# Kernel tuning notes

Measured on AMD Instinct MI355X. Metric: run time of the kernel, lower is better.

## Reference

```python
import jax, jax.numpy as jnp
import numpy as np

N = 100000      # nodes
E = 1600000     # edges
G = 256         # graphs in batch
D_IN = 92
D = 64          # out_dim
EPS = 1e-5      # batchnorm eps


def setup_inputs() -> dict:
    key = jax.random.key(0)
    ks = jax.random.split(key, 20)

    def lin_w(k, fan_in, fan_out):
        return jax.random.normal(k, (fan_in, fan_out), jnp.float32) / np.sqrt(fan_in).astype(np.float32)

    inp = {
        "x": jax.random.normal(ks[0], (N, D_IN), jnp.float32),
        "edge_index": jax.random.randint(ks[1], (2, E), 0, N, dtype=jnp.int64),
        "edge_weight": jax.random.uniform(ks[2], (E,), jnp.float32),
        "batch": jnp.sort(jax.random.randint(ks[3], (N,), 0, G, dtype=jnp.int64)),
        # GCNConv layer 0 (in_channels -> out_dim) + BatchNorm
        "W0": lin_w(ks[4], D_IN, D), "b0": jnp.zeros((D,), jnp.float32),
        "g0": jnp.ones((D,), jnp.float32), "beta0": jnp.zeros((D,), jnp.float32),
        # GCNConv layers 1,2 (out_dim -> out_dim) + BatchNorms
        "W1": lin_w(ks[5], D, D), "b1": jnp.zeros((D,), jnp.float32),
        "g1": jnp.ones((D,), jnp.float32), "beta1": jnp.zeros((D,), jnp.float32),
        "W2": lin_w(ks[6], D, D), "b2": jnp.zeros((D,), jnp.float32),
        "g2": jnp.ones((D,), jnp.float32), "beta2": jnp.zeros((D,), jnp.float32),
        # post MLP: Linear(out_dim,100) -> ReLU -> Linear(100,1)
        "Wp1": lin_w(ks[7], D, 100), "bp1": jnp.zeros((100,), jnp.float32),
        "Wp2": lin_w(ks[8], 100, 1), "bp2": jnp.zeros((1,), jnp.float32),
    }
    return inp


def reference(x, edge_index, edge_weight, batch,
              W0, b0, g0, beta0,
              W1, b1, g1, beta1,
              W2, b2, g2, beta2,
              Wp1, bp1, Wp2, bp2):
    n = x.shape[0]
    # --- gcn_norm with self-loops (fill weight 1), symmetric normalization ---
    loop = jnp.arange(n)
    row = jnp.concatenate([edge_index[0], loop])          # source nodes
    col = jnp.concatenate([edge_index[1], loop])          # target nodes
    w = jnp.concatenate([edge_weight, jnp.ones((n,), x.dtype)])
    deg = jax.ops.segment_sum(w, col, num_segments=n)
    dinv = jnp.where(deg > 0, deg ** -0.5, 0.0)
    norm = dinv[row] * w * dinv[col]                      # [E+N]

    def conv(h, W, b):
        h = h @ W                                         # [n, D]
        msg = norm[:, None] * h[row]                      # gather + scale
        return jax.ops.segment_sum(msg, col, num_segments=n) + b

    def bn(h, g, beta):  # training-mode batchnorm over node dim
        mu = h.mean(0)
        var = h.var(0)
        return (h - mu) * jax.lax.rsqrt(var + EPS) * g + beta

    h = jax.nn.relu(bn(conv(x, W0, b0), g0, beta0))
    h = jax.nn.relu(bn(conv(h, W1, b1), g1, beta1))
    h = jax.nn.relu(bn(conv(h, W2, b2), g2, beta2))

    # global_mean_pool over graph ids
    sums = jax.ops.segment_sum(h, batch, num_segments=G)
    cnt = jax.ops.segment_sum(jnp.ones((n,), h.dtype), batch, num_segments=G)
    pooled = sums / jnp.clip(cnt, 1.0)[:, None]           # [G, D]

    return jax.nn.relu(pooled @ Wp1 + bp1) @ Wp2 + bp2    # [G, 1]
```

## Files before the change

kernel.cpp:

```cpp
#include <hip/hip_runtime.h>
#include <hip/hip_bf16.h>

#define NGRAPH 256
#define BNEPS 1e-5f
#define SEGCAP 64
#define BSHIFT 9
#define BSPAN  512
#define BCAP   10240
#define BSTRIDE 16384
#define GSTAT  8192

typedef short s16x8 __attribute__((ext_vector_type(8)));
typedef float f32x4 __attribute__((ext_vector_type(4)));

__device__ __forceinline__ float bf2f(unsigned short u) {
    return __uint_as_float(((unsigned)u) << 16);
}
__device__ __forceinline__ unsigned short f2bf(float f) {
    unsigned u = __float_as_uint(f);
    unsigned r = (u + 0x7FFFu + ((u >> 16) & 1u)) >> 16;
    return (unsigned short)r;
}

__global__ __launch_bounds__(256) void k_part(const int* __restrict__ row, const int* __restrict__ col,
                                              const float* __restrict__ w,
                                              int* __restrict__ gcur,
                                              float2* __restrict__ stage, int E, int NB) {
    __shared__ int lhist[256];
    __shared__ int lbase[256];
    int tid = threadIdx.x;
    if (tid < NB) lhist[tid] = 0;
    __syncthreads();
    int c[8], lp[8];
    int base = blockIdx.x * 2048;
    #pragma unroll
    for (int k = 0; k < 8; ++k) {
        int e = base + k * 256 + tid;
        c[k] = (e < E) ? col[e] : -1;
        lp[k] = (c[k] >= 0) ? atomicAdd(&lhist[c[k] >> BSHIFT], 1) : 0;
    }
    __syncthreads();
    if (tid < NB && lhist[tid] > 0) lbase[tid] = atomicAdd(&gcur[tid], lhist[tid]);
    __syncthreads();
    #pragma unroll
    for (int k = 0; k < 8; ++k) {
        int e = base + k * 256 + tid;
        if (c[k] < 0) continue;
        int b = c[k] >> BSHIFT;
        int doff = c[k] & (BSPAN - 1);
        int src = row[e];
        float we = w[e];
        int pos = lbase[b] + lp[k];
        if (pos < BCAP)
            stage[(size_t)b * BCAP + pos] =
                make_float2(__int_as_float((doff << 17) | src), we);
    }
}

__global__ __launch_bounds__(256) void k_place(const int* __restrict__ gcur,
                                               const float2* __restrict__ stage,
                                               int* __restrict__ rowptr,
                                               int* __restrict__ cntArr,
                                               float2* __restrict__ edata,
                                               float* __restrict__ dinv, int N) {
    __shared__ int lhist[512];
    __shared__ int lexcl[512];
    __shared__ int lcur[512];
    __shared__ float lwsum[512];
    __shared__ int lts[256];
    int b = blockIdx.x;
    int tid = threadIdx.x;
    int cnt = min(gcur[b], BCAP);
    lhist[tid] = 0; lhist[tid + 256] = 0;
    lcur[tid] = 0;  lcur[tid + 256] = 0;
    lwsum[tid] = 0.0f; lwsum[tid + 256] = 0.0f;
    __syncthreads();
    for (int i = tid; i < cnt; i += 256) {
        unsigned u = __float_as_uint(stage[(size_t)b * BCAP + i].x);
        atomicAdd(&lhist[u >> 17], 1);
    }
    __syncthreads();
    int c0 = (lhist[2 * tid] + 7) & ~7;
    int c1 = (lhist[2 * tid + 1] + 7) & ~7;
    int tsum = c0 + c1;
    lts[tid] = tsum;
    __syncthreads();
    for (int o = 1; o < 256; o <<= 1) {
        int t = (tid >= o) ? lts[tid - o] : 0;
        __syncthreads();
        lts[tid] += t;
        __syncthreads();
    }
    int excl = lts[tid] - tsum;
    lexcl[2 * tid] = excl;
    lexcl[2 * tid + 1] = excl + c0;
    __syncthreads();
    int base = b * BSTRIDE;
    for (int i = tid; i < 512; i += 256) {
        int node = (b << BSHIFT) + i;
        if (node < N) { rowptr[node] = base + lexcl[i]; cntArr[node] = lhist[i]; }
    }
    for (int i = tid; i < cnt; i += 256) {
        float2 p = stage[(size_t)b * BCAP + i];
        unsigned u = __float_as_uint(p.x);
        int doff = (int)(u >> 17);
        int src  = (int)(u & 0x1FFFFu);
        int lp = atomicAdd(&lcur[doff], 1);
        atomicAdd(&lwsum[doff], p.y);
        int pos = lexcl[doff] + lp;
        if (pos < BSTRIDE)
            edata[(size_t)base + pos] = make_float2(__int_as_float(src), p.y);
    }
    __syncthreads();
    for (int i = tid; i < 512; i += 256) {
        int node = (b << BSHIFT) + i;
        if (node < N) dinv[node] = rsqrtf(1.0f + lwsum[i]);
        int c = lhist[i];
        int e8 = (c + 7) & ~7;
        int st = lexcl[i];
        for (int j = c; j < e8; ++j) {
            int pos = st + j;
            if (pos < BSTRIDE) edata[(size_t)base + pos] = make_float2(0.0f, 0.0f);
        }
    }
}

template<int K, bool FUSE_BN>
__global__ __launch_bounds__(256) void k_gemm_m(const float* __restrict__ Hin,
                                                const float* __restrict__ W,
                                                const float* __restrict__ stats,
                                                const float* __restrict__ g,
                                                const float* __restrict__ beta,
                                                const float* __restrict__ dinv,
                                                unsigned short* __restrict__ H2b, int n, float inv_n) {
    constexpr int KP = (K + 31) & ~31;
    constexpr int PITCH = KP + 8;
    __shared__ unsigned short lX[64 * PITCH];
    __shared__ unsigned short lWt[64 * PITCH];
    __shared__ float lmu[64], lsc[64], lbe[64], ldv[64];
    int tid = threadIdx.x;
    int base = blockIdx.x * 64;
    if (FUSE_BN) {
        if (tid < 64) {
            float mu  = stats[tid] * inv_n;
            float var = stats[64 + tid] * inv_n - mu * mu;
            lmu[tid] = mu;
            lsc[tid] = g[tid] * rsqrtf(var + BNEPS);
            lbe[tid] = beta[tid];
        }
        __syncthreads();
    }
    if (tid < 64) {
        int node = base + tid;
        ldv[tid] = (node < n) ? dinv[node] : 0.0f;
    }
    constexpr int XF4 = K / 4;
    for (int idx = tid; idx < 64 * XF4; idx += 256) {
        int nl = idx / XF4;
        int k4 = (idx - nl * XF4) * 4;
        int node = base + nl;
        float4 v = make_float4(0.0f, 0.0f, 0.0f, 0.0f);
        if (node < n) v = *(const float4*)&Hin[(size_t)node * K + k4];
        if (FUSE_BN) {
            v.x = fmaxf((v.x - lmu[k4 + 0]) * lsc[k4 + 0] + lbe[k4 + 0], 0.0f);
            v.y = fmaxf((v.y - lmu[k4 + 1]) * lsc[k4 + 1] + lbe[k4 + 1], 0.0f);
            v.z = fmaxf((v.z - lmu[k4 + 2]) * lsc[k4 + 2] + lbe[k4 + 2], 0.0f);
            v.w = fmaxf((v.w - lmu[k4 + 3]) * lsc[k4 + 3] + lbe[k4 + 3], 0.0f);
        }
        ushort4 pk;
        pk.x = f2bf(v.x); pk.y = f2bf(v.y); pk.z = f2bf(v.z); pk.w = f2bf(v.w);
        *(ushort4*)&lX[nl * PITCH + k4] = pk;
    }
    if constexpr (KP > K) {
        for (int idx = tid; idx < 64 * (KP - K); idx += 256) {
            int nl = idx / (KP - K);
            int kk = K + idx - nl * (KP - K);
            lX[nl * PITCH + kk] = 0;
        }
    }
    for (int idx = tid; idx < K * 16; idx += 256) {
        int kk = idx >> 4;
        int d4 = (idx & 15) * 4;
        float4 v = *(const float4*)&W[(size_t)kk * 64 + d4];
        lWt[(d4 + 0) * PITCH + kk] = f2bf(v.x);
        lWt[(d4 + 1) * PITCH + kk] = f2bf(v.y);
        lWt[(d4 + 2) * PITCH + kk] = f2bf(v.z);
        lWt[(d4 + 3) * PITCH + kk] = f2bf(v.w);
    }
    if constexpr (KP > K) {
        for (int idx = tid; idx < 64 * (KP - K); idx += 256) {
            int dl = idx / (KP - K);
            int kk = K + idx - dl * (KP - K);
            lWt[dl * PITCH + kk] = 0;
        }
    }
    __syncthreads();

    int w = tid >> 6, lane = tid & 63;
    int lrow = lane & 15, kb = lane >> 4;
    f32x4 acc0 = {0.0f, 0.0f, 0.0f, 0.0f};
    f32x4 acc1 = {0.0f, 0.0f, 0.0f, 0.0f};
    f32x4 acc2 = {0.0f, 0.0f, 0.0f, 0.0f};
    f32x4 acc3 = {0.0f, 0.0f, 0.0f, 0.0f};
    #pragma unroll
    for (int k0 = 0; k0 < KP; k0 += 32) {
        int ko = k0 + kb * 8;
        s16x8 a  = *(const s16x8*)&lX[(w * 16 + lrow) * PITCH + ko];
        s16x8 b0 = *(const s16x8*)&lWt[(0  + lrow) * PITCH + ko];
        s16x8 b1 = *(const s16x8*)&lWt[(16 + lrow) * PITCH + ko];
        s16x8 b2 = *(const s16x8*)&lWt[(32 + lrow) * PITCH + ko];
        s16x8 b3 = *(const s16x8*)&lWt[(48 + lrow) * PITCH + ko];
        acc0 = __builtin_amdgcn_mfma_f32_16x16x32_bf16(a, b0, acc0, 0, 0, 0);
        acc1 = __builtin_amdgcn_mfma_f32_16x16x32_bf16(a, b1, acc1, 0, 0, 0);
        acc2 = __builtin_amdgcn_mfma_f32_16x16x32_bf16(a, b2, acc2, 0, 0, 0);
        acc3 = __builtin_amdgcn_mfma_f32_16x16x32_bf16(a, b3, acc3, 0, 0, 0);
    }
    int nrow0 = w * 16 + kb * 4;
    #pragma unroll
    for (int r = 0; r < 4; ++r) {
        int node = base + nrow0 + r;
        if (node < n) {
            float dv = ldv[nrow0 + r];
            size_t rb = (size_t)node * 64;
            H2b[rb + 0  + lrow] = f2bf(acc0[r] * dv);
            H2b[rb + 16 + lrow] = f2bf(acc1[r] * dv);
            H2b[rb + 32 + lrow] = f2bf(acc2[r] * dv);
            H2b[rb + 48 + lrow] = f2bf(acc3[r] * dv);
        }
    }
}

__device__ __forceinline__ void unit8(const float2* __restrict__ segh, int p, unsigned d2,
                                      const unsigned short* __restrict__ Hb,
                                      float& ax, float& ay) {
    float2 e0 = segh[p];
    float2 e1 = segh[p + 2];
    float2 e2 = segh[p + 4];
    float2 e3 = segh[p + 6];
    unsigned o0 = (((unsigned)__float_as_int(e0.x)) << 6) + d2;
    unsigned o1 = (((unsigned)__float_as_int(e1.x)) << 6) + d2;
    unsigned o2 = (((unsigned)__float_as_int(e2.x)) << 6) + d2;
    unsigned o3 = (((unsigned)__float_as_int(e3.x)) << 6) + d2;
    unsigned u0 = *(const unsigned*)&Hb[o0];
    unsigned u1 = *(const unsigned*)&Hb[o1];
    unsigned u2 = *(const unsigned*)&Hb[o2];
    unsigned u3 = *(const unsigned*)&Hb[o3];
    ax = fmaf(e0.y, __uint_as_float(u0 << 16), ax);
    ay = fmaf(e0.y, __uint_as_float(u0 & 0xFFFF0000u), ay);
    ax = fmaf(e1.y, __uint_as_float(u1 << 16), ax);
    ay = fmaf(e1.y, __uint_as_float(u1 & 0xFFFF0000u), ay);
    ax = fmaf(e2.y, __uint_as_float(u2 << 16), ax);
    ay = fmaf(e2.y, __uint_as_float(u2 & 0xFFFF0000u), ay);
    ax = fmaf(e3.y, __uint_as_float(u3 << 16), ax);
    ay = fmaf(e3.y, __uint_as_float(u3 & 0xFFFF0000u), ay);
}

__global__ __launch_bounds__(256) void k_gather(const int* __restrict__ rowptr,
                                                const int* __restrict__ cntArr,
                                                const float2* __restrict__ edata,
                                                const unsigned short* __restrict__ Hb,
                                                const float* __restrict__ b,
                                                const float* __restrict__ dinv,
                                                float* __restrict__ AGG,
                                                float* __restrict__ part, int n, int G) {
    int lane = threadIdx.x & 63;
    int half = lane >> 5;
    unsigned d2 = (unsigned)(lane & 31) * 2;
    int wid = blockIdx.x * 4 + (threadIdx.x >> 6);
    float sx = 0.0f, sy = 0.0f, qx = 0.0f, qy = 0.0f;

    for (int nA = wid * 2; nA < n; nA += G * 8) {
        int nB = nA + 1;
        bool hasB = (nB < n);
        int e8A = ((min(cntArr[nA], SEGCAP) + 7) & ~7);
        int e8B = hasB ? ((min(cntArr[nB], SEGCAP) + 7) & ~7) : 0;
        const float2* shA = edata + rowptr[nA] + half;
        const float2* shB = hasB ? (edata + rowptr[nB] + half) : shA;
        float axA = 0.0f, ayA = 0.0f, axB = 0.0f, ayB = 0.0f;
        int uA = e8A >> 3, uB = e8B >> 3;
        int uc = min(uA, uB);
        int pA = 0, pB = 0;
        for (int t = 0; t < uc; ++t) {
            unit8(shA, pA, d2, Hb, axA, ayA); pA += 8;
            unit8(shB, pB, d2, Hb, axB, ayB); pB += 8;
        }
        for (; pA < e8A; pA += 8) unit8(shA, pA, d2, Hb, axA, ayA);
        for (; pB < e8B; pB += 8) unit8(shB, pB, d2, Hb, axB, ayB);

        axA += __shfl_xor(axA, 32, 64);
        ayA += __shfl_xor(ayA, 32, 64);
        axB += __shfl_xor(axB, 32, 64);
        ayB += __shfl_xor(ayB, 32, 64);
        if (half == 0) {
            {
                unsigned us = *(const unsigned*)&Hb[((unsigned)nA << 6) + d2];
                float ax = axA + __uint_as_float(us << 16);
                float ay = ayA + __uint_as_float(us & 0xFFFF0000u);
                float dv = dinv[nA];
                float2 bb = *(const float2*)&b[d2];
                float2 r;
                r.x = fmaf(dv, ax, bb.x);
                r.y = fmaf(dv, ay, bb.y);
                *(float2*)&AGG[((size_t)nA << 6) + d2] = r;
                sx += r.x; sy += r.y;
                qx = fmaf(r.x, r.x, qx); qy = fmaf(r.y, r.y, qy);
            }
            if (hasB) {
                unsigned us = *(const unsigned*)&Hb[((unsigned)nB << 6) + d2];
                float ax = axB + __uint_as_float(us << 16);
                float ay = ayB + __uint_as_float(us & 0xFFFF0000u);
                float dv = dinv[nB];
                float2 bb = *(const float2*)&b[d2];
                float2 r;
                r.x = fmaf(dv, ax, bb.x);
                r.y = fmaf(dv, ay, bb.y);
                *(float2*)&AGG[((size_t)nB << 6) + d2] = r;
                sx += r.x; sy += r.y;
                qx = fmaf(r.x, r.x, qx); qy = fmaf(r.y, r.y, qy);
            }
        }
    }

    __shared__ float lred[4][64];
    __shared__ float lq[4][64];
    int w = threadIdx.x >> 6;
    if (half == 0) {
        lred[w][d2] = sx; lred[w][d2 + 1] = sy;
        lq[w][d2] = qx;   lq[w][d2 + 1] = qy;
    }
    __syncthreads();
    if (threadIdx.x < 64) {
        int j = threadIdx.x;
        float s = lred[0][j] + lred[1][j] + lred[2][j] + lred[3][j];
        float q = lq[0][j] + lq[1][j] + lq[2][j] + lq[3][j];
        size_t pb = (size_t)blockIdx.x * 128;
        part[pb + j] = s;
        part[pb + 64 + j] = q;
    }
}

__global__ __launch_bounds__(256) void k_red(const float* __restrict__ part,
                                             float* __restrict__ stats, int G) {
    int s = blockIdx.x;
    float v = 0.0f;
    for (int t = threadIdx.x; t < G; t += 256) v += part[(size_t)t * 128 + s];
    __shared__ float l[256];
    l[threadIdx.x] = v;
    __syncthreads();
    for (int o = 128; o > 0; o >>= 1) {
        if (threadIdx.x < o) l[threadIdx.x] += l[threadIdx.x + o];
        __syncthreads();
    }
    if (threadIdx.x == 0) stats[s] = l[0];
}

__global__ __launch_bounds__(256) void k_pool_mlp(const float* __restrict__ AGG,
                                                  const float* __restrict__ stats,
                                                  const float* __restrict__ g,
                                                  const float* __restrict__ beta,
                                                  const int* __restrict__ batch, int n,
                                                  const float* __restrict__ Wp1,
                                                  const float* __restrict__ bp1,
                                                  const float* __restrict__ Wp2,
                                                  const float* __restrict__ bp2,
                                                  float* __restrict__ out, float inv_n) {
    __shared__ float lmu[64], lsc[64], lbe[64];
    int j = threadIdx.x;
    if (j < 64) {
        float mu  = stats[j] * inv_n;
        float var = stats[64 + j] * inv_n - mu * mu;
        lmu[j] = mu;
        lsc[j] = g[j] * rsqrtf(var + BNEPS);
        lbe[j] = beta[j];
    }
    __syncthreads();

    int gidx = blockIdx.x;
    int lo = 0, hi = n;
    while (lo < hi) { int mid = (lo + hi) >> 1; if (batch[mid] < gidx) lo = mid + 1; else hi = mid; }
    int start = lo;
    lo = start; hi = n;
    while (lo < hi) { int mid = (lo + hi) >> 1; if (batch[mid] < gidx + 1) lo = mid + 1; else hi = mid; }
    int end = lo;

    int d = threadIdx.x & 63, grp = threadIdx.x >> 6;
    float s = 0.0f;
    for (int r = start + grp; r < end; r += 4) {
        float v = AGG[(size_t)r * 64 + d];
        s += fmaxf((v - lmu[d]) * lsc[d] + lbe[d], 0.0f);
    }
    __shared__ float ls[256];
    __shared__ float pooled[64];
    ls[threadIdx.x] = s;
    __syncthreads();
    if (grp == 0) {
        float cnt = (float)(end - start);
        float denom = fmaxf(cnt, 1.0f);
        pooled[d] = (ls[d] + ls[64 + d] + ls[128 + d] + ls[192 + d]) / denom;
    }
    __syncthreads();
    __shared__ float hidden[100];
    if (j < 100) {
        float h = bp1[j];
        #pragma unroll 8
        for (int dd = 0; dd < 64; ++dd) h += pooled[dd] * Wp1[dd * 100 + j];
        hidden[j] = fmaxf(h, 0.0f);
    }
    __syncthreads();
    __shared__ float red[256];
    red[j] = (j < 100) ? hidden[j] * Wp2[j] : 0.0f;
    __syncthreads();
    for (int sft = 128; sft > 0; sft >>= 1) {
        if (j < sft) red[j] += red[j + sft];
        __syncthreads();
    }
    if (j == 0) out[gidx] = red[0] + bp2[0];
}

extern "C" void kernel_launch(void* const* d_in, const int* in_sizes, int n_in,
                              void* d_out, int out_size, void* d_ws, size_t ws_size,
                              hipStream_t stream) {
    const float* x    = (const float*)d_in[0];
    const int*   eidx = (const int*)d_in[1];
    const float* ew   = (const float*)d_in[2];
    const int*   batch= (const int*)d_in[3];
    const float* W0 = (const float*)d_in[4];  const float* b0 = (const float*)d_in[5];
    const float* g0 = (const float*)d_in[6];  const float* be0= (const float*)d_in[7];
    const float* W1 = (const float*)d_in[8];  const float* b1 = (const float*)d_in[9];
    const float* g1 = (const float*)d_in[10]; const float* be1= (const float*)d_in[11];
    const float* W2 = (const float*)d_in[12]; const float* b2 = (const float*)d_in[13];
    const float* g2 = (const float*)d_in[14]; const float* be2= (const float*)d_in[15];
    const float* Wp1= (const float*)d_in[16]; const float* bp1= (const float*)d_in[17];
    const float* Wp2= (const float*)d_in[18]; const float* bp2= (const float*)d_in[19];
    float* out = (float*)d_out;

    const int N = in_sizes[3];
    const int E = in_sizes[2];
    const int* row = eidx;
    const int* col = eidx + E;
    const int NB = (N + BSPAN - 1) >> BSHIFT;

    size_t off = 0;
    auto alloc = [&](size_t bytes) {
        void* p = (char*)d_ws + off;
        off += (bytes + 255) & ~(size_t)255;
        return p;
    };
    int*    rowptr = (int*)alloc((size_t)N * 4);
    int*    cntArr = (int*)alloc((size_t)N * 4);
    int*    gcur   = (int*)alloc((size_t)NB * 4);
    float*  dinv   = (float*)alloc((size_t)N * 4);
    float2* stage  = (float2*)alloc((size_t)NB * BCAP * 8);
    float2* edata  = (float2*)alloc((size_t)NB * BSTRIDE * 8);
    unsigned short* H2b = (unsigned short*)alloc((size_t)N * 64 * 2);
    float*  AGG    = (float*)alloc((size_t)N * 64 * 4);
    float*  part   = (float*)alloc((size_t)128 * GSTAT * 4);
    float*  stats  = (float*)alloc(512);
    (void)ws_size;

    const int TB = 256;
    const int gPart = (E + 2047) / 2048;
    const int gGemm = (N + 63) / 64;
    const float inv_n = 1.0f / (float)N;

    hipMemsetAsync(gcur, 0, (size_t)NB * 4, stream);
    k_part<<<gPart, TB, 0, stream>>>(row, col, ew, gcur, stage, E, NB);
    k_place<<<NB, TB, 0, stream>>>(gcur, stage, rowptr, cntArr, edata, dinv, N);

    k_gemm_m<92, false><<<gGemm, TB, 0, stream>>>(x, W0, nullptr, nullptr, nullptr, dinv, H2b, N, inv_n);
    k_gather<<<GSTAT, TB, 0, stream>>>(rowptr, cntArr, edata, H2b, b0, dinv, AGG, part, N, GSTAT);
    k_red<<<128, TB, 0, stream>>>(part, stats, GSTAT);

    k_gemm_m<64, true><<<gGemm, TB, 0, stream>>>(AGG, W1, stats, g0, be0, dinv, H2b, N, inv_n);
    k_gather<<<GSTAT, TB, 0, stream>>>(rowptr, cntArr, edata, H2b, b1, dinv, AGG, part, N, GSTAT);
    k_red<<<128, TB, 0, stream>>>(part, stats, GSTAT);

    k_gemm_m<64, true><<<gGemm, TB, 0, stream>>>(AGG, W2, stats, g1, be1, dinv, H2b, N, inv_n);
    k_gather<<<GSTAT, TB, 0, stream>>>(rowptr, cntArr, edata, H2b, b2, dinv, AGG, part, N, GSTAT);
    k_red<<<128, TB, 0, stream>>>(part, stats, GSTAT);

    k_pool_mlp<<<NGRAPH, TB, 0, stream>>>(AGG, stats, g2, be2, batch, N,
                                          Wp1, bp1, Wp2, bp2, out, inv_n);

    (void)n_in; (void)out_size;
}
```

Measured before the change: 332.0 us.

## Pack edge records into 32-bit words and store aggregates in bf16

Edge records are packed into one 32-bit word: a 17-bit source index plus a truncated 15-bit bf16 weight. This halves edge-stream traffic in each gather, and each half-wave now reads a contiguous half of the segment with 128-bit loads. The per-layer aggregate buffer is stored as bf16 instead of fp32, halving its write and read traffic in the next GEMM and in pooling. The cost is lower precision in edge weights and intermediate activations, and the weight encoding assumes non-negative weights.

After: 298.6 us. 10.1% less time.

```diff
diff --git a/kernel.cpp b/kernel.cpp
--- a/kernel.cpp
+++ b/kernel.cpp
@@ -61,7 +61,7 @@
                                                const float2* __restrict__ stage,
                                                int* __restrict__ rowptr,
                                                int* __restrict__ cntArr,
-                                               float2* __restrict__ edata,
+                                               unsigned* __restrict__ edata,
                                                float* __restrict__ dinv, int N) {
     __shared__ int lhist[512];
     __shared__ int lexcl[512];
@@ -104,12 +104,12 @@
         float2 p = stage[(size_t)b * BCAP + i];
         unsigned u = __float_as_uint(p.x);
         int doff = (int)(u >> 17);
-        int src  = (int)(u & 0x1FFFFu);
+        unsigned src = u & 0x1FFFFu;
         int lp = atomicAdd(&lcur[doff], 1);
         atomicAdd(&lwsum[doff], p.y);
         int pos = lexcl[doff] + lp;
         if (pos < BSTRIDE)
-            edata[(size_t)base + pos] = make_float2(__int_as_float(src), p.y);
+            edata[(size_t)base + pos] = (src << 15) | (unsigned)f2bf(p.y);
     }
     __syncthreads();
     for (int i = tid; i < 512; i += 256) {
@@ -120,13 +120,13 @@
         int st = lexcl[i];
         for (int j = c; j < e8; ++j) {
             int pos = st + j;
-            if (pos < BSTRIDE) edata[(size_t)base + pos] = make_float2(0.0f, 0.0f);
-        }
-    }
-}
-
-template<int K, bool FUSE_BN>
-__global__ __launch_bounds__(256) void k_gemm_m(const float* __restrict__ Hin,
+            if (pos < BSTRIDE) edata[(size_t)base + pos] = 0u;
+        }
+    }
+}
+
+template<int K, bool FUSE_BN, bool IN_BF16>
+__global__ __launch_bounds__(256) void k_gemm_m(const void* __restrict__ HinV,
                                                 const float* __restrict__ W,
                                                 const float* __restrict__ stats,
                                                 const float* __restrict__ g,
@@ -154,22 +154,47 @@
         int node = base + tid;
         ldv[tid] = (node < n) ? dinv[node] : 0.0f;
     }
-    constexpr int XF4 = K / 4;
-    for (int idx = tid; idx < 64 * XF4; idx += 256) {
-        int nl = idx / XF4;
-        int k4 = (idx - nl * XF4) * 4;
-        int node = base + nl;
-        float4 v = make_float4(0.0f, 0.0f, 0.0f, 0.0f);
-        if (node < n) v = *(const float4*)&Hin[(size_t)node * K + k4];
-        if (FUSE_BN) {
-            v.x = fmaxf((v.x - lmu[k4 + 0]) * lsc[k4 + 0] + lbe[k4 + 0], 0.0f);
-            v.y = fmaxf((v.y - lmu[k4 + 1]) * lsc[k4 + 1] + lbe[k4 + 1], 0.0f);
-            v.z = fmaxf((v.z - lmu[k4 + 2]) * lsc[k4 + 2] + lbe[k4 + 2], 0.0f);
-            v.w = fmaxf((v.w - lmu[k4 + 3]) * lsc[k4 + 3] + lbe[k4 + 3], 0.0f);
-        }
-        ushort4 pk;
-        pk.x = f2bf(v.x); pk.y = f2bf(v.y); pk.z = f2bf(v.z); pk.w = f2bf(v.w);
-        *(ushort4*)&lX[nl * PITCH + k4] = pk;
+    if (IN_BF16) {
+        const unsigned short* Hin = (const unsigned short*)HinV;
+        constexpr int U8 = K / 8;
+        for (int idx = tid; idx < 64 * U8; idx += 256) {
+            int nl = idx / U8;
+            int k8 = (idx - nl * U8) * 8;
+            int node = base + nl;
+            ushort4 a = make_ushort4(0, 0, 0, 0), c = make_ushort4(0, 0, 0, 0);
+            if (node < n) {
+                a = *(const ushort4*)&Hin[(size_t)node * K + k8];
+                c = *(const ushort4*)&Hin[(size_t)node * K + k8 + 4];
+            }
+            unsigned short v[8] = {a.x, a.y, a.z, a.w, c.x, c.y, c.z, c.w};
+            #pragma unroll
+            for (int j = 0; j < 8; ++j) {
+                float f = bf2f(v[j]);
+                if (FUSE_BN) f = fmaxf((f - lmu[k8 + j]) * lsc[k8 + j] + lbe[k8 + j], 0.0f);
+                v[j] = f2bf(f);
+            }
+            #pragma unroll
+            for (int j = 0; j < 8; ++j) lX[nl * PITCH + k8 + j] = v[j];
+        }
+    } else {
+        const float* Hin = (const float*)HinV;
+        constexpr int XF4 = K / 4;
+        for (int idx = tid; idx < 64 * XF4; idx += 256) {
+            int nl = idx / XF4;
+            int k4 = (idx - nl * XF4) * 4;
+            int node = base + nl;
+            float4 v = make_float4(0.0f, 0.0f, 0.0f, 0.0f);
+            if (node < n) v = *(const float4*)&Hin[(size_t)node * K + k4];
+            if (FUSE_BN) {
+                v.x = fmaxf((v.x - lmu[k4 + 0]) * lsc[k4 + 0] + lbe[k4 + 0], 0.0f);
+                v.y = fmaxf((v.y - lmu[k4 + 1]) * lsc[k4 + 1] + lbe[k4 + 1], 0.0f);
+                v.z = fmaxf((v.z - lmu[k4 + 2]) * lsc[k4 + 2] + lbe[k4 + 2], 0.0f);
+                v.w = fmaxf((v.w - lmu[k4 + 3]) * lsc[k4 + 3] + lbe[k4 + 3], 0.0f);
+            }
+            ushort4 pk;
+            pk.x = f2bf(v.x); pk.y = f2bf(v.y); pk.z = f2bf(v.z); pk.w = f2bf(v.w);
+            *(ushort4*)&lX[nl * PITCH + k4] = pk;
+        }
     }
     if constexpr (KP > K) {
         for (int idx = tid; idx < 64 * (KP - K); idx += 256) {
@@ -230,38 +255,39 @@
     }
 }
 
-__device__ __forceinline__ void unit8(const float2* __restrict__ segh, int p, unsigned d2,
+__device__ __forceinline__ void unit4(const unsigned* __restrict__ segh, int p, unsigned d2,
                                       const unsigned short* __restrict__ Hb,
                                       float& ax, float& ay) {
-    float2 e0 = segh[p];
-    float2 e1 = segh[p + 2];
-    float2 e2 = segh[p + 4];
-    float2 e3 = segh[p + 6];
-    unsigned o0 = (((unsigned)__float_as_int(e0.x)) << 6) + d2;
-    unsigned o1 = (((unsigned)__float_as_int(e1.x)) << 6) + d2;
-    unsigned o2 = (((unsigned)__float_as_int(e2.x)) << 6) + d2;
-    unsigned o3 = (((unsigned)__float_as_int(e3.x)) << 6) + d2;
+    uint4 q = *(const uint4*)&segh[p];
+    unsigned o0 = ((q.x >> 15) << 6) + d2;
+    unsigned o1 = ((q.y >> 15) << 6) + d2;
+    unsigned o2 = ((q.z >> 15) << 6) + d2;
+    unsigned o3 = ((q.w >> 15) << 6) + d2;
+    float w0 = __uint_as_float((q.x & 0x7FFFu) << 16);
+    float w1 = __uint_as_float((q.y & 0x7FFFu) << 16);
+    float w2 = __uint_as_float((q.z & 0x7FFFu) << 16);
+    float w3 = __uint_as_float((q.w & 0x7FFFu) << 16);
     unsigned u0 = *(const unsigned*)&Hb[o0];
     unsigned u1 = *(const unsigned*)&Hb[o1];
     unsigned u2 = *(const unsigned*)&Hb[o2];
     unsigned u3 = *(const unsigned*)&Hb[o3];
-    ax = fmaf(e0.y, __uint_as_float(u0 << 16), ax);
-    ay = fmaf(e0.y, __uint_as_float(u0 & 0xFFFF0000u), ay);
-    ax = fmaf(e1.y, __uint_as_float(u1 << 16), ax);
-    ay = fmaf(e1.y, __uint_as_float(u1 & 0xFFFF0000u), ay);
-    ax = fmaf(e2.y, __uint_as_float(u2 << 16), ax);
-    ay = fmaf(e2.y, __uint_as_float(u2 & 0xFFFF0000u), ay);
-    ax = fmaf(e3.y, __uint_as_float(u3 << 16), ax);
-    ay = fmaf(e3.y, __uint_as_float(u3 & 0xFFFF0000u), ay);
+    ax = fmaf(w0, __uint_as_float(u0 << 16), ax);
+    ay = fmaf(w0, __uint_as_float(u0 & 0xFFFF0000u), ay);
+    ax = fmaf(w1, __uint_as_float(u1 << 16), ax);
+    ay = fmaf(w1, __uint_as_float(u1 & 0xFFFF0000u), ay);
+    ax = fmaf(w2, __uint_as_float(u2 << 16), ax);
+    ay = fmaf(w2, __uint_as_float(u2 & 0xFFFF0000u), ay);
+    ax = fmaf(w3, __uint_as_float(u3 << 16), ax);
+    ay = fmaf(w3, __uint_as_float(u3 & 0xFFFF0000u), ay);
 }
 
 __global__ __launch_bounds__(256) void k_gather(const int* __restrict__ rowptr,
                                                 const int* __restrict__ cntArr,
-                                                const float2* __restrict__ edata,
+                                                const unsigned* __restrict__ edata,
                                                 const unsigned short* __restrict__ Hb,
                                                 const float* __restrict__ b,
                                                 const float* __restrict__ dinv,
-                                                float* __restrict__ AGG,
+                                                unsigned short* __restrict__ AGGb,
                                                 float* __restrict__ part, int n, int G) {
     int lane = threadIdx.x & 63;
     int half = lane >> 5;
@@ -272,20 +298,19 @@
     for (int nA = wid * 2; nA < n; nA += G * 8) {
         int nB = nA + 1;
         bool hasB = (nB < n);
-        int e8A = ((min(cntArr[nA], SEGCAP) + 7) & ~7);
-        int e8B = hasB ? ((min(cntArr[nB], SEGCAP) + 7) & ~7) : 0;
-        const float2* shA = edata + rowptr[nA] + half;
-        const float2* shB = hasB ? (edata + rowptr[nB] + half) : shA;
+        int ehA = ((min(cntArr[nA], SEGCAP) + 7) & ~7) >> 1;
+        int ehB = hasB ? (((min(cntArr[nB], SEGCAP) + 7) & ~7) >> 1) : 0;
+        const unsigned* shA = edata + rowptr[nA] + half * ehA;
+        const unsigned* shB = hasB ? (edata + rowptr[nB] + half * ehB) : shA;
         float axA = 0.0f, ayA = 0.0f, axB = 0.0f, ayB = 0.0f;
-        int uA = e8A >> 3, uB = e8B >> 3;
-        int uc = min(uA, uB);
+        int uc = min(ehA, ehB);
         int pA = 0, pB = 0;
-        for (int t = 0; t < uc; ++t) {
-            unit8(shA, pA, d2, Hb, axA, ayA); pA += 8;
-            unit8(shB, pB, d2, Hb, axB, ayB); pB += 8;
-        }
-        for (; pA < e8A; pA += 8) unit8(shA, pA, d2, Hb, axA, ayA);
-        for (; pB < e8B; pB += 8) unit8(shB, pB, d2, Hb, axB, ayB);
+        for (; pA < uc; pA += 4, pB += 4) {
+            unit4(shA, pA, d2, Hb, axA, ayA);
+            unit4(shB, pB, d2, Hb, axB, ayB);
+        }
+        for (; pA < ehA; pA += 4) unit4(shA, pA, d2, Hb, axA, ayA);
+        for (; pB < ehB; pB += 4) unit4(shB, pB, d2, Hb, axB, ayB);
 
         axA += __shfl_xor(axA, 32, 64);
         ayA += __shfl_xor(ayA, 32, 64);
@@ -298,12 +323,12 @@
                 float ay = ayA + __uint_as_float(us & 0xFFFF0000u);
                 float dv = dinv[nA];
                 float2 bb = *(const float2*)&b[d2];
-                float2 r;
-                r.x = fmaf(dv, ax, bb.x);
-                r.y = fmaf(dv, ay, bb.y);
-                *(float2*)&AGG[((size_t)nA << 6) + d2] = r;
-                sx += r.x; sy += r.y;
-                qx = fmaf(r.x, r.x, qx); qy = fmaf(r.y, r.y, qy);
+                float rx = fmaf(dv, ax, bb.x);
+                float ry = fmaf(dv, ay, bb.y);
+                unsigned pk = (unsigned)f2bf(rx) | ((unsigned)f2bf(ry) << 16);
+                *(unsigned*)&AGGb[((size_t)nA << 6) + d2] = pk;
+                sx += rx; sy += ry;
+                qx = fmaf(rx, rx, qx); qy = fmaf(ry, ry, qy);
             }
             if (hasB) {
                 unsigned us = *(const unsigned*)&Hb[((unsigned)nB << 6) + d2];
@@ -311,12 +336,12 @@
                 float ay = ayB + __uint_as_float(us & 0xFFFF0000u);
                 float dv = dinv[nB];
                 float2 bb = *(const float2*)&b[d2];
-                float2 r;
-                r.x = fmaf(dv, ax, bb.x);
-                r.y = fmaf(dv, ay, bb.y);
-                *(float2*)&AGG[((size_t)nB << 6) + d2] = r;
-                sx += r.x; sy += r.y;
-                qx = fmaf(r.x, r.x, qx); qy = fmaf(r.y, r.y, qy);
+                float rx = fmaf(dv, ax, bb.x);
+                float ry = fmaf(dv, ay, bb.y);
+                unsigned pk = (unsigned)f2bf(rx) | ((unsigned)f2bf(ry) << 16);
+                *(unsigned*)&AGGb[((size_t)nB << 6) + d2] = pk;
+                sx += rx; sy += ry;
+                qx = fmaf(rx, rx, qx); qy = fmaf(ry, ry, qy);
             }
         }
     }
@@ -354,7 +379,7 @@
     if (threadIdx.x == 0) stats[s] = l[0];
 }
 
-__global__ __launch_bounds__(256) void k_pool_mlp(const float* __restrict__ AGG,
+__global__ __launch_bounds__(256) void k_pool_mlp(const unsigned short* __restrict__ AGGb,
                                                   const float* __restrict__ stats,
                                                   const float* __restrict__ g,
                                                   const float* __restrict__ beta,
@@ -386,7 +411,7 @@
     int d = threadIdx.x & 63, grp = threadIdx.x >> 6;
     float s = 0.0f;
     for (int r = start + grp; r < end; r += 4) {
-        float v = AGG[(size_t)r * 64 + d];
+        float v = bf2f(AGGb[(size_t)r * 64 + d]);
         s += fmaxf((v - lmu[d]) * lsc[d] + lbe[d], 0.0f);
     }
     __shared__ float ls[256];
@@ -446,16 +471,16 @@
         off += (bytes + 255) & ~(size_t)255;
         return p;
     };
-    int*    rowptr = (int*)alloc((size_t)N * 4);
-    int*    cntArr = (int*)alloc((size_t)N * 4);
-    int*    gcur   = (int*)alloc((size_t)NB * 4);
-    float*  dinv   = (float*)alloc((size_t)N * 4);
-    float2* stage  = (float2*)alloc((size_t)NB * BCAP * 8);
-    float2* edata  = (float2*)alloc((size_t)NB * BSTRIDE * 8);
-    unsigned short* H2b = (unsigned short*)alloc((size_t)N * 64 * 2);
-    float*  AGG    = (float*)alloc((size_t)N * 64 * 4);
-    float*  part   = (float*)alloc((size_t)128 * GSTAT * 4);
-    float*  stats  = (float*)alloc(512);
+    int*      rowptr = (int*)alloc((size_t)N * 4);
+    int*      cntArr = (int*)alloc((size_t)N * 4);
+    int*      gcur   = (int*)alloc((size_t)NB * 4);
+    float*    dinv   = (float*)alloc((size_t)N * 4);
+    float2*   stage  = (float2*)alloc((size_t)NB * BCAP * 8);
+    unsigned* edata  = (unsigned*)alloc((size_t)NB * BSTRIDE * 4);
+    unsigned short* H2b  = (unsigned short*)alloc((size_t)N * 64 * 2);
+    unsigned short* AGGb = (unsigned short*)alloc((size_t)N * 64 * 2);
+    float*    part   = (float*)alloc((size_t)128 * GSTAT * 4);
+    float*    stats  = (float*)alloc(512);
     (void)ws_size;
 
     const int TB = 256;
@@ -467,19 +492,19 @@
     k_part<<<gPart, TB, 0, stream>>>(row, col, ew, gcur, stage, E, NB);
     k_place<<<NB, TB, 0, stream>>>(gcur, stage, rowptr, cntArr, edata, dinv, N);
 
-    k_gemm_m<92, false><<<gGemm, TB, 0, stream>>>(x, W0, nullptr, nullptr, nullptr, dinv, H2b, N, inv_n);
-    k_gather<<<GSTAT, TB, 0, stream>>>(rowptr, cntArr, edata, H2b, b0, dinv, AGG, part, N, GSTAT);
+    k_gemm_m<92, false, false><<<gGemm, TB, 0, stream>>>(x, W0, nullptr, nullptr, nullptr, dinv, H2b, N, inv_n);
+    k_gather<<<GSTAT, TB, 0, stream>>>(rowptr, cntArr, edata, H2b, b0, dinv, AGGb, part, N, GSTAT);
     k_red<<<128, TB, 0, stream>>>(part, stats, GSTAT);
 
-    k_gemm_m<64, true><<<gGemm, TB, 0, stream>>>(AGG, W1, stats, g0, be0, dinv, H2b, N, inv_n);
-    k_gather<<<GSTAT, TB, 0, stream>>>(rowptr, cntArr, edata, H2b, b1, dinv, AGG, part, N, GSTAT);
+    k_gemm_m<64, true, true><<<gGemm, TB, 0, stream>>>(AGGb, W1, stats, g0, be0, dinv, H2b, N, inv_n);
+    k_gather<<<GSTAT, TB, 0, stream>>>(rowptr, cntArr, edata, H2b, b1, dinv, AGGb, part, N, GSTAT);
     k_red<<<128, TB, 0, stream>>>(part, stats, GSTAT);
 
-    k_gemm_m<64, true><<<gGemm, TB, 0, stream>>>(AGG, W2, stats, g1, be1, dinv, H2b, N, inv_n);
-    k_gather<<<GSTAT, TB, 0, stream>>>(rowptr, cntArr, edata, H2b, b2, dinv, AGG, part, N, GSTAT);
+    k_gemm_m<64, true, true><<<gGemm, TB, 0, stream>>>(AGGb, W2, stats, g1, be1, dinv, H2b, N, inv_n);
+    k_gather<<<GSTAT, TB, 0, stream>>>(rowptr, cntArr, edata, H2b, b2, dinv, AGGb, part, N, GSTAT);
     k_red<<<128, TB, 0, stream>>>(part, stats, GSTAT);
 
-    k_pool_mlp<<<NGRAPH, TB, 0, stream>>>(AGG, stats, g2, be2, batch, N,
+    k_pool_mlp<<<NGRAPH, TB, 0, stream>>>(AGGb, stats, g2, be2, batch, N,
                                           Wp1, bp1, Wp2, bp2, out, inv_n);
 
     (void)n_in; (void)out_size;
```
